# Kernel optimization log

Hardware: AMD Instinct MI355X
Metric: run time of the kernel (lower is better)

The kernel has to match this reference:

```python
import jax, jax.numpy as jnp
import numpy as np

B, N, C = 4, 2048, 320
H, D = 5, 64            # heads, dim_head
INNER = H * D           # 320


def setup_inputs() -> dict:
    key = jax.random.key(0)
    ks = jax.random.split(key, 7)
    x = jax.random.normal(ks[0], (B, N, C), dtype=jnp.float32)
    edge = jax.random.uniform(ks[1], (B, N, 1), dtype=jnp.float32)
    s = 1.0 / np.sqrt(C)
    Wq = jax.random.normal(ks[2], (C, INNER), dtype=jnp.float32) * s
    Wk = jax.random.normal(ks[3], (C, INNER), dtype=jnp.float32) * s
    Wv = jax.random.normal(ks[4], (C, INNER), dtype=jnp.float32) * s
    Wo = jax.random.normal(ks[5], (INNER, C), dtype=jnp.float32) * (1.0 / np.sqrt(INNER))
    bo = jnp.zeros((C,), dtype=jnp.float32)
    return {"x": x, "edge": edge, "Wq": Wq, "Wk": Wk, "Wv": Wv, "Wo": Wo, "bo": bo}


def _split_heads(t):
    # 'b n (h d) -> (b h) n d'  (batch-major, head-minor)
    b, n, _ = t.shape
    return t.reshape(b, n, H, D).transpose(0, 2, 1, 3).reshape(b * H, n, D)


def reference(x, edge, Wq, Wk, Wv, Wo, bo):
    scale = D ** -0.5
    q = _split_heads(x @ Wq).astype(jnp.float32)   # (B*H, N, D)
    k = _split_heads(x @ Wk).astype(jnp.float32)
    v = _split_heads(x @ Wv)

    sim = jnp.einsum('bid,bjd->bij', q, k) * scale  # (B*H, N, N)

    # torch: edge.repeat(h, 1, 1) -> batch-minor tiling; index i uses edge[i % B]
    edge_rep = jnp.tile(edge, (H, 1, 1))            # (H*B, N, 1)
    edge_matrix = edge_rep * edge_rep.transpose(0, 2, 1)  # outer product (H*B, N, N)

    sim = jax.nn.softmax(sim * edge_matrix, axis=-1)
    out = jnp.einsum('bij,bjd->bid', sim, v)        # (B*H, N, D)

    # '(b h) n d -> b n (h d)'
    out = out.reshape(B, H, N, D).transpose(0, 2, 1, 3).reshape(B, N, INNER)
    return out @ Wo + bo
```

## Files before the change

kernel.cpp:

```cpp
#include <hip/hip_runtime.h>
#include <hip/hip_bf16.h>
#include <math.h>


typedef short bf16x8 __attribute__((ext_vector_type(8)));
typedef float f32x4 __attribute__((ext_vector_type(4)));

static __device__ __forceinline__ ushort f2bf(float f) {
  union { float f; unsigned u; } v; v.f = f;
  unsigned r = (v.u + 0x7fffu + ((v.u >> 16) & 1u)) >> 16;
  return (ushort)r;
}
static __device__ __forceinline__ float fexp2(float x) {
#if __has_builtin(__builtin_amdgcn_exp2f)
  return __builtin_amdgcn_exp2f(x);
#else
  return exp2f(x);
#endif
}
static __device__ __forceinline__ f32x4 mfma32(bf16x8 a, bf16x8 b, f32x4 c) {
  return __builtin_amdgcn_mfma_f32_16x16x32_bf16(a, b, c, 0, 0, 0);
}

__global__ __launch_bounds__(256) void xcvt_kernel(
    const float* __restrict__ x, ushort* __restrict__ xb)
{
  const int t = threadIdx.x;
  const int mt2 = blockIdx.x;
  const int kc = blockIdx.y * 2 + (t >> 7);
  const int f = (t & 127) * 4;
  const int qq = f >> 7, mm = (f >> 3) & 15, e0 = f & 7;
  float4 v = *reinterpret_cast<const float4*>(
      x + (size_t)(mt2 * 16 + mm) * 320 + kc * 32 + qq * 8 + e0);
  ushort4 o = { f2bf(v.x), f2bf(v.y), f2bf(v.z), f2bf(v.w) };
  *reinterpret_cast<ushort4*>(xb + (size_t)(mt2 * 10 + kc) * 512 + f) = o;
}

__global__ __launch_bounds__(256) void wtrans_kernel(
    const float* __restrict__ Wq, const float* __restrict__ Wk,
    const float* __restrict__ Wv, const float* __restrict__ Wo,
    ushort* __restrict__ wt)
{
  const int z = blockIdx.z;
  const float* W = z == 0 ? Wq : z == 1 ? Wk : z == 2 ? Wv : Wo;
  const int nt2 = blockIdx.x, kc = blockIdx.y;
  const int f = threadIdx.x * 2;
  const int qq = f >> 7, nn = (f >> 3) & 15, e0 = f & 7;
  const int k = kc * 32 + qq * 8 + e0, n = nt2 * 16 + nn;
  float v0 = W[(size_t)k * 320 + n];
  float v1 = W[(size_t)(k + 1) * 320 + n];
  ushort2 o = { f2bf(v0), f2bf(v1) };
  *reinterpret_cast<ushort2*>(
      wt + (size_t)z * 102400 + (size_t)(nt2 * 10 + kc) * 512 + f) = o;
}

__global__ __launch_bounds__(256, 4) void qkv_gemm(
    const ushort* __restrict__ xb, const float* __restrict__ edge,
    const ushort* __restrict__ wt,
    ushort* __restrict__ qp, ushort* __restrict__ kS, ushort* __restrict__ vS)
{
  const int w = blockIdx.x;
  const int s = (w & 7) * 60 + (w >> 3);
  const int mg = s / 15, zh = s % 15;
  const int z = zh / 5, h = zh % 5;
  const int wave = threadIdx.x >> 6, lane = threadIdx.x & 63;
  const int m16 = lane & 15, quad = lane >> 4;
  const int m0 = mg * 256 + wave * 64;
  const int row16 = m0 >> 4;
  const ushort* atile = xb + (size_t)row16 * 5120 + lane * 8;
  const ushort* btile = wt + (size_t)z * 102400 + (size_t)(h * 4) * 5120 + lane * 8;

  f32x4 acc[4][4];
#pragma unroll
  for (int i = 0; i < 4; ++i)
#pragma unroll
    for (int ns = 0; ns < 4; ++ns) acc[i][ns] = (f32x4){0.f, 0.f, 0.f, 0.f};

#pragma unroll
  for (int kc = 0; kc < 10; ++kc) {
    bf16x8 af[4], bf[4];
#pragma unroll
    for (int i = 0; i < 4; ++i)
      af[i] = *reinterpret_cast<const bf16x8*>(atile + (i * 10 + kc) * 512);
#pragma unroll
    for (int ns = 0; ns < 4; ++ns)
      bf[ns] = *reinterpret_cast<const bf16x8*>(btile + (ns * 10 + kc) * 512);
#pragma unroll
    for (int i = 0; i < 4; ++i)
#pragma unroll
      for (int ns = 0; ns < 4; ++ns)
        acc[i][ns] = mfma32(af[i], bf[ns], acc[i][ns]);
  }

  const float QSCALE = 0.18033688011112042f;
  const int b = m0 >> 11;
  const int bh = b * 5 + h;
  const float* eb = edge + (size_t)((b + h) & 3) * 2048;
  const int nwb = m0 & 2047;

  if (z == 0) {
#pragma unroll
    for (int i = 0; i < 4; ++i) {
      const int nb = nwb + i * 16 + quad * 4;
      float e[4];
#pragma unroll
      for (int r = 0; r < 4; ++r) e[r] = eb[nb + r] * QSCALE;
      ushort* dst = qp + ((size_t)bh * 2048 + nb) * 64;
#pragma unroll
      for (int ns = 0; ns < 4; ++ns)
#pragma unroll
        for (int r = 0; r < 4; ++r)
          dst[(size_t)r * 64 + ns * 16 + m16] = f2bf(acc[i][ns][r] * e[r]);
    }
  } else if (z == 1) {
#pragma unroll
    for (int i = 0; i < 4; ++i) {
      const int nb = nwb + i * 16 + quad * 4;
      float e[4];
#pragma unroll
      for (int r = 0; r < 4; ++r) e[r] = eb[nb + r];
      const int j16 = ((m0 >> 4) + i) & 127;
      const size_t base = (size_t)bh * 131072 + (size_t)j16 * 1024;
#pragma unroll
      for (int ns = 0; ns < 4; ++ns) {
        size_t a0 = base + (ns >> 1) * 512 +
                    (((ns & 1) * 2 + (m16 >> 3)) * 16 + quad * 4) * 8 + (m16 & 7);
#pragma unroll
        for (int r = 0; r < 4; ++r)
          kS[a0 + (size_t)r * 8] = f2bf(acc[i][ns][r] * e[r]);
      }
    }
  } else {
    const int jb = nwb >> 6;
#pragma unroll
    for (int i = 0; i < 4; ++i) {
      const int kb = i >> 1, e4 = (i & 1) * 4;
#pragma unroll
      for (int ns = 0; ns < 4; ++ns) {
        ushort4 o = { f2bf(acc[i][ns][0]), f2bf(acc[i][ns][1]),
                      f2bf(acc[i][ns][2]), f2bf(acc[i][ns][3]) };
        size_t addr = (size_t)bh * 131072 + (size_t)ns * 32768 +
                      (size_t)jb * 1024 + kb * 512 +
                      (quad * 16 + m16) * 8 + e4;
        *reinterpret_cast<ushort4*>(vS + addr) = o;
      }
    }
  }
}

__global__ __launch_bounds__(256, 2) void attn_kernel(
    const ushort* __restrict__ qp, const ushort* __restrict__ kS,
    const ushort* __restrict__ vS, ushort* __restrict__ ao)
{
  __shared__ f32x4 lo[3][8][64];
  __shared__ float lrs[4][2][16];
  const int w = blockIdx.x;
  const int s = (w & 7) * 160 + (w >> 3);
  const int bh = s >> 6, qt = s & 63;
  const int b = bh / 5, h = bh % 5;
  const int wave = threadIdx.x >> 6, lane = threadIdx.x & 63;
  const int m16 = lane & 15, quad = lane >> 4;
  const int q0 = qt * 32;

  bf16x8 qf[2][2];
#pragma unroll
  for (int qs = 0; qs < 2; ++qs) {
    const ushort* qrow = qp + ((size_t)bh * 2048 + q0 + qs * 16 + m16) * 64;
    qf[qs][0] = *reinterpret_cast<const bf16x8*>(qrow + quad * 8);
    qf[qs][1] = *reinterpret_cast<const bf16x8*>(qrow + 32 + quad * 8);
  }
  const ushort* kb_p = kS + (size_t)bh * 131072 + lane * 8;
  const ushort* vb_p = vS + (size_t)bh * 131072 + lane * 8;

  f32x4 oacc[2][4], rsacc[2];
#pragma unroll
  for (int qs = 0; qs < 2; ++qs) {
    rsacc[qs] = (f32x4){0.f, 0.f, 0.f, 0.f};
    for (int dt = 0; dt < 4; ++dt) oacc[qs][dt] = (f32x4){0.f, 0.f, 0.f, 0.f};
  }
  const bf16x8 ones8 = {(short)16256, (short)16256, (short)16256, (short)16256,
                        (short)16256, (short)16256, (short)16256, (short)16256};

  auto load_unit = [&](int u, bf16x8 kf[2][2], bf16x8 vf[4]) {
    const int jb = (u >> 1) * 4 + wave, kb = u & 1;
#pragma unroll
    for (int ss = 0; ss < 2; ++ss)
#pragma unroll
      for (int hf = 0; hf < 2; ++hf)
        kf[ss][hf] = *reinterpret_cast<const bf16x8*>(
            kb_p + (size_t)(jb * 4 + kb * 2 + ss) * 1024 + hf * 512);
#pragma unroll
    for (int dt = 0; dt < 4; ++dt)
      vf[dt] = *reinterpret_cast<const bf16x8*>(
          vb_p + (size_t)dt * 32768 + (size_t)jb * 1024 + kb * 512);
  };
  auto compute_unit = [&](bf16x8 kf[2][2], bf16x8 vf[4]) {
#pragma unroll
    for (int qs = 0; qs < 2; ++qs) {
      f32x4 st0 = (f32x4){0.f, 0.f, 0.f, 0.f};
      f32x4 st1 = (f32x4){0.f, 0.f, 0.f, 0.f};
      st0 = mfma32(kf[0][0], qf[qs][0], st0);
      st0 = mfma32(kf[0][1], qf[qs][1], st0);
      st1 = mfma32(kf[1][0], qf[qs][0], st1);
      st1 = mfma32(kf[1][1], qf[qs][1], st1);
      unsigned b0 = __float_as_uint(fexp2(st0[0]));
      unsigned b1 = __float_as_uint(fexp2(st0[1]));
      unsigned b2 = __float_as_uint(fexp2(st0[2]));
      unsigned b3 = __float_as_uint(fexp2(st0[3]));
      unsigned b4 = __float_as_uint(fexp2(st1[0]));
      unsigned b5 = __float_as_uint(fexp2(st1[1]));
      unsigned b6 = __float_as_uint(fexp2(st1[2]));
      unsigned b7 = __float_as_uint(fexp2(st1[3]));
      union { unsigned u[4]; bf16x8 v; } pk;
      pk.u[0] = __builtin_amdgcn_perm(b1, b0, 0x07060302u);
      pk.u[1] = __builtin_amdgcn_perm(b3, b2, 0x07060302u);
      pk.u[2] = __builtin_amdgcn_perm(b5, b4, 0x07060302u);
      pk.u[3] = __builtin_amdgcn_perm(b7, b6, 0x07060302u);
      rsacc[qs] = mfma32(ones8, pk.v, rsacc[qs]);
#pragma unroll
      for (int dt = 0; dt < 4; ++dt)
        oacc[qs][dt] = mfma32(vf[dt], pk.v, oacc[qs][dt]);
    }
  };

  bf16x8 kA[2][2], vA[4], kB[2][2], vB[4];
  load_unit(0, kA, vA);
  __builtin_amdgcn_sched_barrier(0);
#pragma unroll
  for (int u = 0; u < 16; u += 2) {
    load_unit(u + 1, kB, vB);
    __builtin_amdgcn_sched_barrier(0);
    compute_unit(kA, vA);
    if (u + 2 < 16) load_unit(u + 2, kA, vA);
    __builtin_amdgcn_sched_barrier(0);
    compute_unit(kB, vB);
    __builtin_amdgcn_sched_barrier(0);
  }

  if (wave > 0) {
#pragma unroll
    for (int qs = 0; qs < 2; ++qs)
#pragma unroll
      for (int dt = 0; dt < 4; ++dt)
        lo[wave - 1][qs * 4 + dt][lane] = oacc[qs][dt];
  }
  if (quad == 0) {
    lrs[wave][0][m16] = rsacc[0][0];
    lrs[wave][1][m16] = rsacc[1][0];
  }
  __syncthreads();
  if (wave == 0) {
#pragma unroll
    for (int qs = 0; qs < 2; ++qs) {
      float inv = 1.0f / (lrs[0][qs][m16] + lrs[1][qs][m16] +
                          lrs[2][qs][m16] + lrs[3][qs][m16]);
      const int mt2 = b * 128 + qt * 2 + qs;
#pragma unroll
      for (int dt = 0; dt < 4; ++dt) {
        f32x4 a = oacc[qs][dt];
        a += lo[0][qs * 4 + dt][lane];
        a += lo[1][qs * 4 + dt][lane];
        a += lo[2][qs * 4 + dt][lane];
        unsigned r0 = f2bf(a[0] * inv), r1 = f2bf(a[1] * inv);
        unsigned r2 = f2bf(a[2] * inv), r3 = f2bf(a[3] * inv);
        uint2 ww;
        ww.x = r0 | (r1 << 16);
        ww.y = r2 | (r3 << 16);
        size_t addr = (size_t)(mt2 * 10 + h * 2 + (dt >> 1)) * 512 +
                      ((((dt & 1) * 2 + (quad >> 1)) * 16 + m16)) * 8 +
                      (quad & 1) * 4;
        *reinterpret_cast<uint2*>(ao + addr) = ww;
      }
    }
  }
}

__global__ __launch_bounds__(128, 4) void oproj_gemm(
    const ushort* __restrict__ ao, const ushort* __restrict__ wt,
    const float* __restrict__ bo, float* __restrict__ out)
{
  const int w = blockIdx.x;
  const int s = (w & 7) * 40 + (w >> 3);
  const int mg = s / 5, ct = s % 5;
  const int wave = threadIdx.x >> 6, lane = threadIdx.x & 63;
  const int m16 = lane & 15, quad = lane >> 4;
  const int m0 = mg * 128 + wave * 64;
  const int n0 = ct * 64;
  const ushort* atile = ao + (size_t)(m0 >> 4) * 5120 + lane * 8;
  const ushort* btile = wt + (size_t)3 * 102400 + (size_t)(ct * 4) * 5120 + lane * 8;

  f32x4 acc[4][4];
#pragma unroll
  for (int i = 0; i < 4; ++i)
#pragma unroll
    for (int ns = 0; ns < 4; ++ns) acc[i][ns] = (f32x4){0.f, 0.f, 0.f, 0.f};

#pragma unroll
  for (int kc = 0; kc < 10; ++kc) {
    bf16x8 af[4], bf[4];
#pragma unroll
    for (int i = 0; i < 4; ++i)
      af[i] = *reinterpret_cast<const bf16x8*>(atile + (i * 10 + kc) * 512);
#pragma unroll
    for (int ns = 0; ns < 4; ++ns)
      bf[ns] = *reinterpret_cast<const bf16x8*>(btile + (ns * 10 + kc) * 512);
#pragma unroll
    for (int i = 0; i < 4; ++i)
#pragma unroll
      for (int ns = 0; ns < 4; ++ns)
        acc[i][ns] = mfma32(af[i], bf[ns], acc[i][ns]);
  }

  float bb[4];
#pragma unroll
  for (int ns = 0; ns < 4; ++ns) bb[ns] = bo[n0 + ns * 16 + m16];
#pragma unroll
  for (int i = 0; i < 4; ++i) {
    const int mrow = m0 + i * 16 + quad * 4;
#pragma unroll
    for (int ns = 0; ns < 4; ++ns)
#pragma unroll
      for (int r = 0; r < 4; ++r)
        out[(size_t)(mrow + r) * 320 + n0 + ns * 16 + m16] = acc[i][ns][r] + bb[ns];
  }
}

extern "C" void kernel_launch(void* const* d_in, const int* in_sizes, int n_in,
                              void* d_out, int out_size, void* d_ws, size_t ws_size,
                              hipStream_t stream) {
  const float* x    = (const float*)d_in[0];
  const float* edge = (const float*)d_in[1];
  const float* Wq   = (const float*)d_in[2];
  const float* Wk   = (const float*)d_in[3];
  const float* Wv   = (const float*)d_in[4];
  const float* Wo   = (const float*)d_in[5];
  const float* bo   = (const float*)d_in[6];
  float* out = (float*)d_out;

  ushort* xb = (ushort*)d_ws;
  ushort* wt = xb + (size_t)8192 * 320;
  ushort* qp = wt + (size_t)4 * 320 * 320;
  ushort* kS = qp + (size_t)20 * 2048 * 64;
  ushort* vS = kS + (size_t)20 * 2048 * 64;
  ushort* ao = vS + (size_t)20 * 2048 * 64;

  xcvt_kernel<<<dim3(512, 5), 256, 0, stream>>>(x, xb);
  wtrans_kernel<<<dim3(20, 10, 4), 256, 0, stream>>>(Wq, Wk, Wv, Wo, wt);
  qkv_gemm<<<480, 256, 0, stream>>>(xb, edge, wt, qp, kS, vS);
  attn_kernel<<<1280, 256, 0, stream>>>(qp, kS, vS, ao);
  oproj_gemm<<<320, 128, 0, stream>>>(ao, wt, bo, out);
}
```

Baseline: 134.0 us.

## Merge prep kernels, swap MFMA operands for vectorized epilogue stores, retune occupancy

Fuses the x conversion and weight transposition kernels into one launch, saving a kernel launch. Swaps the MFMA A/B operands in the Q/K projections and the output projection so each lane holds four contiguous columns, letting the epilogues use ushort4 and float4 stores instead of scalar scattered stores. Also changes the launch-bounds occupancy hints (qkv 4->3, attn 2->3), which shifts register budgets and risks spills or lower occupancy.

```diff
diff --git a/kernel.cpp b/kernel.cpp
--- a/kernel.cpp
+++ b/kernel.cpp
@@ -22,39 +22,39 @@
   return __builtin_amdgcn_mfma_f32_16x16x32_bf16(a, b, c, 0, 0, 0);
 }
 
-__global__ __launch_bounds__(256) void xcvt_kernel(
-    const float* __restrict__ x, ushort* __restrict__ xb)
-{
-  const int t = threadIdx.x;
-  const int mt2 = blockIdx.x;
-  const int kc = blockIdx.y * 2 + (t >> 7);
-  const int f = (t & 127) * 4;
-  const int qq = f >> 7, mm = (f >> 3) & 15, e0 = f & 7;
-  float4 v = *reinterpret_cast<const float4*>(
-      x + (size_t)(mt2 * 16 + mm) * 320 + kc * 32 + qq * 8 + e0);
-  ushort4 o = { f2bf(v.x), f2bf(v.y), f2bf(v.z), f2bf(v.w) };
-  *reinterpret_cast<ushort4*>(xb + (size_t)(mt2 * 10 + kc) * 512 + f) = o;
-}
-
-__global__ __launch_bounds__(256) void wtrans_kernel(
+__global__ __launch_bounds__(256) void prep_kernel(
+    const float* __restrict__ x,
     const float* __restrict__ Wq, const float* __restrict__ Wk,
     const float* __restrict__ Wv, const float* __restrict__ Wo,
-    ushort* __restrict__ wt)
+    ushort* __restrict__ xb, ushort* __restrict__ wt)
 {
-  const int z = blockIdx.z;
-  const float* W = z == 0 ? Wq : z == 1 ? Wk : z == 2 ? Wv : Wo;
-  const int nt2 = blockIdx.x, kc = blockIdx.y;
-  const int f = threadIdx.x * 2;
-  const int qq = f >> 7, nn = (f >> 3) & 15, e0 = f & 7;
-  const int k = kc * 32 + qq * 8 + e0, n = nt2 * 16 + nn;
-  float v0 = W[(size_t)k * 320 + n];
-  float v1 = W[(size_t)(k + 1) * 320 + n];
-  ushort2 o = { f2bf(v0), f2bf(v1) };
-  *reinterpret_cast<ushort2*>(
-      wt + (size_t)z * 102400 + (size_t)(nt2 * 10 + kc) * 512 + f) = o;
-}
-
-__global__ __launch_bounds__(256, 4) void qkv_gemm(
+  const int w = blockIdx.x;
+  if (w < 2560) {
+    const int t = threadIdx.x;
+    const int mt2 = w / 5;
+    const int kc = (w % 5) * 2 + (t >> 7);
+    const int f = (t & 127) * 4;
+    const int qq = f >> 7, mm = (f >> 3) & 15, e0 = f & 7;
+    float4 v = *reinterpret_cast<const float4*>(
+        x + (size_t)(mt2 * 16 + mm) * 320 + kc * 32 + qq * 8 + e0);
+    ushort4 o = { f2bf(v.x), f2bf(v.y), f2bf(v.z), f2bf(v.w) };
+    *reinterpret_cast<ushort4*>(xb + (size_t)(mt2 * 10 + kc) * 512 + f) = o;
+  } else {
+    const int w2 = w - 2560;
+    const int nt2 = w2 % 20, kc = (w2 / 20) % 10, z = w2 / 200;
+    const float* W = z == 0 ? Wq : z == 1 ? Wk : z == 2 ? Wv : Wo;
+    const int f = threadIdx.x * 2;
+    const int qq = f >> 7, nn = (f >> 3) & 15, e0 = f & 7;
+    const int k = kc * 32 + qq * 8 + e0, n = nt2 * 16 + nn;
+    float v0 = W[(size_t)k * 320 + n];
+    float v1 = W[(size_t)(k + 1) * 320 + n];
+    ushort2 o = { f2bf(v0), f2bf(v1) };
+    *reinterpret_cast<ushort2*>(
+        wt + (size_t)z * 102400 + (size_t)(nt2 * 10 + kc) * 512 + f) = o;
+  }
+}
+
+__global__ __launch_bounds__(256, 3) void qkv_gemm(
     const ushort* __restrict__ xb, const float* __restrict__ edge,
     const ushort* __restrict__ wt,
     ushort* __restrict__ qp, ushort* __restrict__ kS, ushort* __restrict__ vS)
@@ -66,8 +66,7 @@
   const int wave = threadIdx.x >> 6, lane = threadIdx.x & 63;
   const int m16 = lane & 15, quad = lane >> 4;
   const int m0 = mg * 256 + wave * 64;
-  const int row16 = m0 >> 4;
-  const ushort* atile = xb + (size_t)row16 * 5120 + lane * 8;
+  const ushort* atile = xb + (size_t)(m0 >> 4) * 5120 + lane * 8;
   const ushort* btile = wt + (size_t)z * 102400 + (size_t)(h * 4) * 5120 + lane * 8;
 
   f32x4 acc[4][4];
@@ -85,11 +84,19 @@
 #pragma unroll
     for (int ns = 0; ns < 4; ++ns)
       bf[ns] = *reinterpret_cast<const bf16x8*>(btile + (ns * 10 + kc) * 512);
-#pragma unroll
-    for (int i = 0; i < 4; ++i)
-#pragma unroll
-      for (int ns = 0; ns < 4; ++ns)
-        acc[i][ns] = mfma32(af[i], bf[ns], acc[i][ns]);
+    if (z == 2) {
+#pragma unroll
+      for (int i = 0; i < 4; ++i)
+#pragma unroll
+        for (int ns = 0; ns < 4; ++ns)
+          acc[i][ns] = mfma32(af[i], bf[ns], acc[i][ns]);
+    } else {
+#pragma unroll
+      for (int i = 0; i < 4; ++i)
+#pragma unroll
+        for (int ns = 0; ns < 4; ++ns)
+          acc[i][ns] = mfma32(bf[ns], af[i], acc[i][ns]);
+    }
   }
 
   const float QSCALE = 0.18033688011112042f;
@@ -101,33 +108,31 @@
   if (z == 0) {
 #pragma unroll
     for (int i = 0; i < 4; ++i) {
-      const int nb = nwb + i * 16 + quad * 4;
-      float e[4];
-#pragma unroll
-      for (int r = 0; r < 4; ++r) e[r] = eb[nb + r] * QSCALE;
-      ushort* dst = qp + ((size_t)bh * 2048 + nb) * 64;
-#pragma unroll
-      for (int ns = 0; ns < 4; ++ns)
-#pragma unroll
-        for (int r = 0; r < 4; ++r)
-          dst[(size_t)r * 64 + ns * 16 + m16] = f2bf(acc[i][ns][r] * e[r]);
+      const int n = nwb + i * 16 + m16;
+      const float e = eb[n] * QSCALE;
+      ushort* dst = qp + ((size_t)bh * 2048 + n) * 64 + quad * 4;
+#pragma unroll
+      for (int ns = 0; ns < 4; ++ns) {
+        ushort4 o = { f2bf(acc[i][ns][0] * e), f2bf(acc[i][ns][1] * e),
+                      f2bf(acc[i][ns][2] * e), f2bf(acc[i][ns][3] * e) };
+        *reinterpret_cast<ushort4*>(dst + ns * 16) = o;
+      }
     }
   } else if (z == 1) {
 #pragma unroll
     for (int i = 0; i < 4; ++i) {
-      const int nb = nwb + i * 16 + quad * 4;
-      float e[4];
-#pragma unroll
-      for (int r = 0; r < 4; ++r) e[r] = eb[nb + r];
-      const int j16 = ((m0 >> 4) + i) & 127;
-      const size_t base = (size_t)bh * 131072 + (size_t)j16 * 1024;
+      const int j = nwb + i * 16 + m16;
+      const float e = eb[j];
+      const size_t base = (size_t)bh * 131072 +
+                          (size_t)((m0 >> 4) + i & 127) * 1024;
 #pragma unroll
       for (int ns = 0; ns < 4; ++ns) {
         size_t a0 = base + (ns >> 1) * 512 +
-                    (((ns & 1) * 2 + (m16 >> 3)) * 16 + quad * 4) * 8 + (m16 & 7);
-#pragma unroll
-        for (int r = 0; r < 4; ++r)
-          kS[a0 + (size_t)r * 8] = f2bf(acc[i][ns][r] * e[r]);
+                    ((((ns * 2 + (quad >> 1)) & 3) * 16 + m16)) * 8 +
+                    (quad & 1) * 4;
+        ushort4 o = { f2bf(acc[i][ns][0] * e), f2bf(acc[i][ns][1] * e),
+                      f2bf(acc[i][ns][2] * e), f2bf(acc[i][ns][3] * e) };
+        *reinterpret_cast<ushort4*>(kS + a0) = o;
       }
     }
   } else {
@@ -148,7 +153,7 @@
   }
 }
 
-__global__ __launch_bounds__(256, 2) void attn_kernel(
+__global__ __launch_bounds__(256, 3) void attn_kernel(
     const ushort* __restrict__ qp, const ushort* __restrict__ kS,
     const ushort* __restrict__ vS, ushort* __restrict__ ao)
 {
@@ -308,20 +313,26 @@
     for (int i = 0; i < 4; ++i)
 #pragma unroll
       for (int ns = 0; ns < 4; ++ns)
-        acc[i][ns] = mfma32(af[i], bf[ns], acc[i][ns]);
-  }
-
-  float bb[4];
-#pragma unroll
-  for (int ns = 0; ns < 4; ++ns) bb[ns] = bo[n0 + ns * 16 + m16];
+        acc[i][ns] = mfma32(bf[ns], af[i], acc[i][ns]);
+  }
+
+  float4 bb[4];
+#pragma unroll
+  for (int ns = 0; ns < 4; ++ns)
+    bb[ns] = *reinterpret_cast<const float4*>(bo + n0 + ns * 16 + quad * 4);
 #pragma unroll
   for (int i = 0; i < 4; ++i) {
-    const int mrow = m0 + i * 16 + quad * 4;
-#pragma unroll
-    for (int ns = 0; ns < 4; ++ns)
-#pragma unroll
-      for (int r = 0; r < 4; ++r)
-        out[(size_t)(mrow + r) * 320 + n0 + ns * 16 + m16] = acc[i][ns][r] + bb[ns];
+    const int mrow = m0 + i * 16 + m16;
+#pragma unroll
+    for (int ns = 0; ns < 4; ++ns) {
+      float4 o;
+      o.x = acc[i][ns][0] + bb[ns].x;
+      o.y = acc[i][ns][1] + bb[ns].y;
+      o.z = acc[i][ns][2] + bb[ns].z;
+      o.w = acc[i][ns][3] + bb[ns].w;
+      *reinterpret_cast<float4*>(
+          out + (size_t)mrow * 320 + n0 + ns * 16 + quad * 4) = o;
+    }
   }
 }
 
@@ -344,8 +355,7 @@
   ushort* vS = kS + (size_t)20 * 2048 * 64;
   ushort* ao = vS + (size_t)20 * 2048 * 64;
 
-  xcvt_kernel<<<dim3(512, 5), 256, 0, stream>>>(x, xb);
-  wtrans_kernel<<<dim3(20, 10, 4), 256, 0, stream>>>(Wq, Wk, Wv, Wo, wt);
+  prep_kernel<<<3360, 256, 0, stream>>>(x, Wq, Wk, Wv, Wo, xb, wt);
   qkv_gemm<<<480, 256, 0, stream>>>(xb, edge, wt, qp, kS, vS);
   attn_kernel<<<1280, 256, 0, stream>>>(qp, kS, vS, ao);
   oproj_gemm<<<320, 128, 0, stream>>>(ao, wt, bo, out);
```

After: 130.6 us. 2.5% less time.
